# Performance work log

Measured on AMD Instinct MI355X. Metric: run time of the kernel, lower is better.

Reference implementation:

```python
import jax, jax.numpy as jnp
import numpy as np

B, T, N, SD, D, HYP, EMB = 128, 256, 8, 200, 64, 64, 32

def _ln(x, g, b, eps=1e-5):
    mu = jnp.mean(x, -1, keepdims=True)
    v = jnp.mean((x - mu) ** 2, -1, keepdims=True)
    return (x - mu) * jax.lax.rsqrt(v + eps) * g + b

def setup_inputs():
    key = jax.random.key(0)
    ks = iter(jax.random.split(key, 64))
    def p(shape, scale=0.05):
        return (jax.random.normal(next(ks), shape) * scale).astype(jnp.float32)
    n, sd, d, hyp, emb = N, SD, D, HYP, EMB
    return dict(
        qvals=p((B, T, n), 1.0), states=p((B, T, sd), 1.0), hidden_state=p((B, T, n, d), 1.0),
        enc_w1=p((sd, d)), enc_b1=p((d,)), enc_w2=p((d, d)), enc_b2=p((d,)),
        wq=p((d, d)), bq=p((d,)), wk=p((d, d)), bk=p((d,)), wv=p((d, d)), bv=p((d,)),
        wo=p((d, d)), bo=p((d,)),
        ln1_g=jnp.ones((d,), jnp.float32), ln1_b=jnp.zeros((d,), jnp.float32),
        ffn_w1=p((d, d)), ffn_b1=p((d,)), ffn_w2=p((d, d)), ffn_b2=p((d,)),
        ln2_g=jnp.ones((d,), jnp.float32), ln2_b=jnp.zeros((d,), jnp.float32),
        fc2ni_w=p((n, d, n - 1)), fc2ni_b=p((n, n - 1)),
        norm_g=jnp.ones((n - 1,), jnp.float32), norm_b=jnp.zeros((n - 1,), jnp.float32),
        w1a=p((2 * d, hyp)), b1a=p((hyp,)), w1b=p((hyp, n * emb)), b1b=p((n * emb,)),
        hb1w=p((2 * d, emb)), hb1b=p((emb,)),
        w2a=p((2 * d, hyp)), b2a=p((hyp,)), w2b=p((hyp, emb)), b2b=p((emb,)),
        hb2w1=p((2 * d, emb)), hb2b1=p((emb,)), hb2w2=p((emb, 1)), hb2b2=p((1,)))

def reference(qvals, states, hidden_state, enc_w1, enc_b1, enc_w2, enc_b2,
              wq, bq, wk, bk, wv, bv, wo, bo, ln1_g, ln1_b,
              ffn_w1, ffn_b1, ffn_w2, ffn_b2, ln2_g, ln2_b,
              fc2ni_w, fc2ni_b, norm_g, norm_b,
              w1a, b1a, w1b, b1b, hb1w, hb1b,
              w2a, b2a, w2b, b2b, hb2w1, hb2b1, hb2w2, hb2b2):
    sg = jax.lax.stop_gradient
    b, t, n = qvals.shape
    bt = b * t
    d = hidden_state.shape[-1]
    emb = hb1w.shape[1]
    # Encoder_s: relu(fc1) then tanh(fc2(e)+e)
    s = states.reshape(bt, -1)
    e = jax.nn.relu(s @ enc_w1 + enc_b1)
    enc = jnp.tanh(e @ enc_w2 + enc_b2 + e)                       # (bt, 64)
    # concat detached agent hiddens with detached state embedding -> (bt, n+1, 64)
    h = jnp.concatenate([sg(hidden_state.reshape(bt, n, d)), sg(enc)[:, None, :]], axis=1)
    # transformer block (single-head self-attention + FFN, post-LN)
    q = h @ wq + bq; k = h @ wk + bk; v = h @ wv + bv
    att = jax.nn.softmax(jnp.einsum('bid,bjd->bij', q, k) / jnp.sqrt(jnp.float32(d)), axis=-1)
    h2 = _ln(h + (att @ v) @ wo + bo, ln1_g, ln1_b)
    h3 = _ln(h2 + jax.nn.relu(h2 @ ffn_w1 + ffn_b1) @ ffn_w2 + ffn_b2, ln2_g, ln2_b)
    h_trans = h3[:, :n]                                           # (bt, n, 64)
    ens = jnp.concatenate([enc, sg(h_trans).mean(1)], axis=-1)    # (bt, 128)
    # per-agent fc2_Ni -> LayerNorm -> sigmoid, vectorized over agents
    ni = jnp.einsum('xnd,nde->xne', h_trans, fc2ni_w) + fc2ni_b   # (bt, n, n-1)
    ni = jax.nn.sigmoid(_ln(ni, norm_g, norm_b))
    # insert 1.0 at the diagonal (agent i keeps its own q with weight 1)
    rows = jnp.arange(n)[:, None]; cols = jnp.arange(n)[None, :]
    gidx = jnp.clip(cols - (cols > rows).astype(jnp.int32), 0, n - 2)  # (n, n)
    gathered = jnp.take_along_axis(ni, jnp.broadcast_to(gidx, (bt, n, n)), axis=-1)
    nfull = jnp.where(cols == rows, jnp.float32(1.0), gathered)   # (bt, n, n)
    N_nn = nfull.reshape(b, t, n, n)
    q_ni = (qvals[:, :, None, :] * N_nn).sum(-1).reshape(bt, 1, n)
    # hypernetwork mixing (QMIX)
    ens_d = sg(ens)
    w1 = jnp.abs(jax.nn.relu(ens_d @ w1a + b1a) @ w1b + b1b).reshape(bt, n, emb)
    b1 = (ens_d @ hb1w + hb1b).reshape(bt, 1, emb)
    w2 = jnp.abs(jax.nn.relu(ens @ w2a + b2a) @ w2b + b2b).reshape(bt, emb, 1)
    b2 = (jax.nn.relu(ens @ hb2w1 + hb2b1) @ hb2w2 + hb2b2).reshape(bt, 1, 1)
    hidden = jax.nn.elu(q_ni @ w1 + b1)
    y = (hidden @ w2 + b2).reshape(b, t, 1)
    eye_mask = jnp.broadcast_to(jnp.eye(n, dtype=bool), (b, t, n, n))
    return y, N_nn, eye_mask
```

## Files before the change

kernel.cpp:

```cpp
#include <hip/hip_runtime.h>
#include <hip/hip_bf16.h>

typedef __bf16 bf16x8 __attribute__((ext_vector_type(8)));
typedef __bf16 bf16x4 __attribute__((ext_vector_type(4)));
typedef float f32x4 __attribute__((ext_vector_type(4)));

#define ROWSG 32768
#define RB 8
#define HPAD 72
#define NN_OFF ((size_t)ROWSG)
#define EYE_OFF ((size_t)ROWSG + (size_t)ROWSG*64)

#define OFF_EW1   0
#define OFF_EW2   14336
#define OFF_WQ    18432
#define OFF_WK    22528
#define OFF_WV    26624
#define OFF_WO    30720
#define OFF_F1    34816
#define OFF_F2    38912
#define OFF_W1A   43008
#define OFF_W1B   51200
#define OFF_HB1W  67584
#define OFF_W2A   71680
#define OFF_W2B   79872
#define OFF_HB2W1 81920
#define WS_TOTAL  86016

__device__ __align__(16) __bf16 g_ws[WS_TOTAL];

#define MFMA16(a,b,c) __builtin_amdgcn_mfma_f32_16x16x32_bf16(a,b,c,0,0,0)

struct TP { const float* src[14]; };

__global__ __launch_bounds__(256) void wtrans(TP tp) {
    const int gid = blockIdx.x * 256 + threadIdx.x;
    if (gid >= WS_TOTAL) return;
    const int OFFS[14] = {OFF_EW1, OFF_EW2, OFF_WQ, OFF_WK, OFF_WV, OFF_WO, OFF_F1,
                          OFF_F2, OFF_W1A, OFF_W1B, OFF_HB1W, OFF_W2A, OFF_W2B, OFF_HB2W1};
    const int KPS[14]  = {224, 64, 64, 64, 64, 64, 64, 64, 128, 64, 128, 128, 64, 128};
    const int KRS[14]  = {200, 64, 64, 64, 64, 64, 64, 64, 128, 64, 128, 128, 64, 128};
    const int NS[14]   = {64, 64, 64, 64, 64, 64, 64, 64, 64, 256, 32, 64, 32, 32};
    int m = 0;
#pragma unroll
    for (int i = 1; i < 14; ++i) if (gid >= OFFS[i]) m = i;
    const int loc = gid - OFFS[m];
    const int Kp = KPS[m];
    const int n = loc / Kp;
    const int k = loc - n * Kp;
    float v = 0.f;
    if (k < KRS[m]) v = tp.src[m][(size_t)k * NS[m] + n];
    g_ws[gid] = (__bf16)v;
}

struct MainP {
    const float *qvals, *states, *hid, *eb1, *eb2, *bq, *bk, *bv, *bo,
        *l1g, *l1b, *fb1, *fb2, *l2g, *l2b, *niw, *nib, *ng, *nb,
        *b1a, *b1b, *hb1b, *b2a, *b2b, *hb2b1, *hw2, *hb2b2;
    float* out;
};

__device__ __forceinline__ void proj_ln(const __bf16* A, const __bf16* WT,
                                        const float* bias, const float* g, const float* bb,
                                        __bf16* H, int w, int quad, int l15) {
    for (int mti = 0; mti < 2; ++mti) {
        const int mt = w + 4 * mti;
        if (mt >= 5) continue;
        f32x4 acc0 = {0,0,0,0}, acc1 = {0,0,0,0}, acc2 = {0,0,0,0}, acc3 = {0,0,0,0};
#pragma unroll
        for (int ks = 0; ks < 2; ++ks) {
            const int kk = ks * 32 + quad * 8;
            const bf16x8 af = *(const bf16x8*)(A + (mt * 16 + l15) * HPAD + kk);
            acc0 = MFMA16(af, *(const bf16x8*)(WT + (size_t)(0 * 16 + l15) * 64 + kk), acc0);
            acc1 = MFMA16(af, *(const bf16x8*)(WT + (size_t)(1 * 16 + l15) * 64 + kk), acc1);
            acc2 = MFMA16(af, *(const bf16x8*)(WT + (size_t)(2 * 16 + l15) * 64 + kk), acc2);
            acc3 = MFMA16(af, *(const bf16x8*)(WT + (size_t)(3 * 16 + l15) * 64 + kk), acc3);
        }
        float v[4][4], g4[4], b4[4];
#pragma unroll
        for (int nt = 0; nt < 4; ++nt) {
            const int col = nt * 16 + l15;
            const float bo = bias[col];
            g4[nt] = g[col]; b4[nt] = bb[col];
            const f32x4 a = (nt == 0) ? acc0 : (nt == 1) ? acc1 : (nt == 2) ? acc2 : acc3;
#pragma unroll
            for (int r = 0; r < 4; ++r)
                v[nt][r] = a[r] + bo + (float)H[(mt * 16 + quad * 4 + r) * HPAD + col];
        }
#pragma unroll
        for (int r = 0; r < 4; ++r) {
            float s  = v[0][r] + v[1][r] + v[2][r] + v[3][r];
            float s2 = v[0][r]*v[0][r] + v[1][r]*v[1][r] + v[2][r]*v[2][r] + v[3][r]*v[3][r];
#pragma unroll
            for (int off = 1; off < 16; off <<= 1) {
                s  += __shfl_xor(s,  off, 64);
                s2 += __shfl_xor(s2, off, 64);
            }
            const float mu  = s * 0.015625f;
            const float var = s2 * 0.015625f - mu * mu;
            const float rs  = rsqrtf(var + 1e-5f);
#pragma unroll
            for (int nt = 0; nt < 4; ++nt)
                H[(mt * 16 + quad * 4 + r) * HPAD + nt * 16 + l15] =
                    (__bf16)((v[nt][r] - mu) * rs * g4[nt] + b4[nt]);
        }
    }
}

__global__ __launch_bounds__(256) void mixer_main(MainP p) {
    __shared__ __align__(16) __bf16 Hb[80 * HPAD];
    __shared__ __align__(16) __bf16 Qb[80 * HPAD];
    __shared__ __align__(16) __bf16 Kb[80 * HPAD];
    __shared__ __align__(16) __bf16 EbU[16 * HPAD];
    __shared__ __align__(16) __bf16 Tb2[16 * HPAD];
    __shared__ __align__(16) __bf16 ensB[16 * 136];
    __shared__ float  attU[8 * 81];
    __shared__ float  sQv[64];
    __shared__ float  qniL[64];
    __shared__ __align__(16) __bf16 W1bS[8 * 256];
    __shared__ float  B1f[8 * 32], W2f[8 * 32], T3f[8 * 32];

    const int blk = blockIdx.x;
    const int bt0 = blk * RB;
    const int t = threadIdx.x;
    const int w = t >> 6, lane = t & 63, quad = lane >> 4, l15 = lane & 15;
    const __bf16* ws = g_ws;
    __bf16* Sb = W1bS;

#pragma unroll
    for (int it = 0; it < 4; ++it) {
        const int u = it * 256 + t;
        const int x = u >> 7, rem = u & 127, n = rem >> 4, d4 = (rem & 15) * 4;
        const float4 v4 = *(const float4*)(p.hid + ((size_t)(bt0 + x) * 512 + n * 64 + d4));
        bf16x4 o; o[0] = (__bf16)v4.x; o[1] = (__bf16)v4.y; o[2] = (__bf16)v4.z; o[3] = (__bf16)v4.w;
        *(bf16x4*)(Hb + (x * 9 + n) * HPAD + d4) = o;
    }
#pragma unroll
    for (int it = 0; it < 2; ++it) {
        const int u = it * 256 + t;
        if (u < 400) {
            const int xr = u / 50, c4 = u - xr * 50;
            const float4 v4 = *(const float4*)(p.states + (size_t)(bt0 + xr) * 200 + c4 * 4);
            bf16x4 o; o[0] = (__bf16)v4.x; o[1] = (__bf16)v4.y; o[2] = (__bf16)v4.z; o[3] = (__bf16)v4.w;
            *(bf16x4*)(Sb + xr * 224 + c4 * 4) = o;
        }
    }
    if (t < 192) { const int xr = t / 24, c = t - xr * 24; Sb[xr * 224 + 200 + c] = (__bf16)0.0f; }
    if (t < 64) sQv[t] = p.qvals[(size_t)(bt0 + (t >> 3)) * 8 + (t & 7)];
    __syncthreads();

    float e4[4];
    {
        const int n0 = w * 16;
        const int srow = (l15 < 8) ? l15 : 7;
        f32x4 acc = {0, 0, 0, 0};
        for (int ks = 0; ks < 7; ++ks) {
            const int kk = ks * 32 + quad * 8;
            const bf16x8 af = *(const bf16x8*)(Sb + srow * 224 + kk);
            const bf16x8 bf = *(const bf16x8*)(ws + OFF_EW1 + (size_t)(n0 + l15) * 224 + kk);
            acc = MFMA16(af, bf, acc);
        }
        const float b1 = p.eb1[n0 + l15];
#pragma unroll
        for (int r = 0; r < 4; ++r) {
            const float ev = fmaxf(acc[r] + b1, 0.f);
            e4[r] = ev;
            EbU[(quad * 4 + r) * HPAD + n0 + l15] = (__bf16)ev;
        }
    }
    __syncthreads();

    {
        const int n0 = w * 16;
        f32x4 acc = {0, 0, 0, 0};
#pragma unroll
        for (int ks = 0; ks < 2; ++ks) {
            const int kk = ks * 32 + quad * 8;
            const bf16x8 af = *(const bf16x8*)(EbU + l15 * HPAD + kk);
            const bf16x8 bf = *(const bf16x8*)(ws + OFF_EW2 + (size_t)(n0 + l15) * 64 + kk);
            acc = MFMA16(af, bf, acc);
        }
        const float b2 = p.eb2[n0 + l15];
#pragma unroll
        for (int r = 0; r < 4; ++r) {
            const int xr = quad * 4 + r;
            if (xr < RB) {
                const float ev = tanhf(acc[r] + e4[r] + b2);
                Hb[(xr * 9 + 8) * HPAD + n0 + l15] = (__bf16)ev;
                ensB[xr * 136 + n0 + l15] = (__bf16)ev;
            }
        }
    }
    __syncthreads();

    for (int it = 0; it < 10; ++it) {
        const int j = w + 4 * it;
        const int mat = j / 20, r20 = j % 20, mt = r20 >> 2, nt = r20 & 3;
        const __bf16* wt = ws + (mat == 0 ? OFF_WQ : OFF_WK);
        const float* bias = (mat == 0 ? p.bq : p.bk);
        __bf16* dst = (mat == 0 ? Qb : Kb);
        f32x4 acc = {0, 0, 0, 0};
#pragma unroll
        for (int ks = 0; ks < 2; ++ks) {
            const int kk = ks * 32 + quad * 8;
            const bf16x8 af = *(const bf16x8*)(Hb + (mt * 16 + l15) * HPAD + kk);
            const bf16x8 bf = *(const bf16x8*)(wt + (size_t)(nt * 16 + l15) * 64 + kk);
            acc = MFMA16(af, bf, acc);
        }
        const float bv = bias[nt * 16 + l15];
#pragma unroll
        for (int r = 0; r < 4; ++r)
            dst[(mt * 16 + quad * 4 + r) * HPAD + nt * 16 + l15] = (__bf16)(acc[r] + bv);
    }
    __syncthreads();

    for (int xi = 0; xi < 2; ++xi) {
        const int x = w * 2 + xi;
        const int arow = (x * 9 + l15) * HPAD;
        f32x4 acc = {0, 0, 0, 0};
#pragma unroll
        for (int ks = 0; ks < 2; ++ks) {
            const int kk = ks * 32 + quad * 8;
            const bf16x8 qa = *(const bf16x8*)(Qb + arow + kk);
            const bf16x8 kb = *(const bf16x8*)(Kb + arow + kk);
            acc = MFMA16(qa, kb, acc);
        }
#pragma unroll
        for (int r = 0; r < 4; ++r) {
            const int i = quad * 4 + r;
            float s = (l15 < 9) ? acc[r] * 0.125f : -3.0e38f;
            float m = s;
#pragma unroll
            for (int off = 1; off < 16; off <<= 1) m = fmaxf(m, __shfl_xor(m, off, 64));
            float e = (l15 < 9) ? __expf(s - m) : 0.f;
            float sum = e;
#pragma unroll
            for (int off = 1; off < 16; off <<= 1) sum += __shfl_xor(sum, off, 64);
            const float pv = e / sum;
            if (i < 9 && l15 < 9) attU[x * 81 + i * 9 + l15] = pv;
        }
    }
    __syncthreads();

    for (int xi = 0; xi < 2; ++xi) {
        const int x = w * 2 + xi;
        float vreg[9];
#pragma unroll
        for (int jj = 0; jj < 9; ++jj) vreg[jj] = (float)Hb[(x * 9 + jj) * HPAD + lane];
#pragma unroll
        for (int i = 0; i < 9; ++i) {
            float a = 0.f;
#pragma unroll
            for (int jj = 0; jj < 9; ++jj) a += attU[x * 81 + i * 9 + jj] * vreg[jj];
            Kb[(x * 9 + i) * HPAD + lane] = (__bf16)a;
        }
    }
    __syncthreads();

    for (int it = 0; it < 5; ++it) {
        const int j = w + 4 * it;
        const int mt = j >> 2, nt = j & 3;
        f32x4 acc = {0, 0, 0, 0};
#pragma unroll
        for (int ks = 0; ks < 2; ++ks) {
            const int kk = ks * 32 + quad * 8;
            const bf16x8 af = *(const bf16x8*)(Kb + (mt * 16 + l15) * HPAD + kk);
            const bf16x8 bf = *(const bf16x8*)(ws + OFF_WV + (size_t)(nt * 16 + l15) * 64 + kk);
            acc = MFMA16(af, bf, acc);
        }
        const float bv = p.bv[nt * 16 + l15];
#pragma unroll
        for (int r = 0; r < 4; ++r)
            Qb[(mt * 16 + quad * 4 + r) * HPAD + nt * 16 + l15] = (__bf16)(acc[r] + bv);
    }
    __syncthreads();

    proj_ln(Qb, ws + OFF_WO, p.bo, p.l1g, p.l1b, Hb, w, quad, l15);
    __syncthreads();

    for (int it = 0; it < 5; ++it) {
        const int j = w + 4 * it;
        const int mt = j >> 2, nt = j & 3;
        f32x4 acc = {0, 0, 0, 0};
#pragma unroll
        for (int ks = 0; ks < 2; ++ks) {
            const int kk = ks * 32 + quad * 8;
            const bf16x8 af = *(const bf16x8*)(Hb + (mt * 16 + l15) * HPAD + kk);
            const bf16x8 bf = *(const bf16x8*)(ws + OFF_F1 + (size_t)(nt * 16 + l15) * 64 + kk);
            acc = MFMA16(af, bf, acc);
        }
        const float fb = p.fb1[nt * 16 + l15];
#pragma unroll
        for (int r = 0; r < 4; ++r)
            Kb[(mt * 16 + quad * 4 + r) * HPAD + nt * 16 + l15] = (__bf16)fmaxf(acc[r] + fb, 0.f);
    }
    __syncthreads();

    proj_ln(Kb, ws + OFF_F2, p.fb2, p.l2g, p.l2b, Hb, w, quad, l15);
    __syncthreads();

#pragma unroll
    for (int it = 0; it < 2; ++it) {
        const int id = it * 256 + t;
        const int x = id >> 6, col = id & 63;
        float s = 0.f;
#pragma unroll
        for (int i = 0; i < 8; ++i) s += (float)Hb[(x * 9 + i) * HPAD + col];
        ensB[x * 136 + 64 + col] = (__bf16)(s * 0.125f);
    }
    __syncthreads();

    {
        const int pr = t >> 2, q4 = t & 3;
        const int x = pr >> 3, n = pr & 7;
        float acc[7] = {0.f, 0.f, 0.f, 0.f, 0.f, 0.f, 0.f};
        const float* wni = p.niw + n * 448;
        for (int dd = 0; dd < 16; ++dd) {
            const int d = q4 * 16 + dd;
            const float hv = (float)Hb[(x * 9 + n) * HPAD + d];
#pragma unroll
            for (int e = 0; e < 7; ++e) acc[e] += hv * wni[d * 7 + e];
        }
#pragma unroll
        for (int e = 0; e < 7; ++e) {
            acc[e] += __shfl_xor(acc[e], 1, 64);
            acc[e] += __shfl_xor(acc[e], 2, 64);
        }
        if (q4 == 0) {
            float s = 0.f;
#pragma unroll
            for (int e = 0; e < 7; ++e) { acc[e] += p.nib[n * 7 + e]; s += acc[e]; }
            const float mu = s * (1.f / 7.f);
            float s2 = 0.f;
#pragma unroll
            for (int e = 0; e < 7; ++e) { const float d0 = acc[e] - mu; s2 += d0 * d0; }
            const float rs = rsqrtf(s2 * (1.f / 7.f) + 1e-5f);
            float* sNi = (float*)EbU;
#pragma unroll
            for (int e = 0; e < 7; ++e) {
                const float vv = (acc[e] - mu) * rs * p.ng[e] + p.nb[e];
                sNi[x * 64 + n * 8 + e] = 1.f / (1.f + __expf(-vv));
            }
        }
    }
    __syncthreads();

    {
        const float* sNi = (const float*)EbU;
        float* Nf = attU;
#pragma unroll
        for (int it = 0; it < 2; ++it) {
            const int id = it * 256 + t;
            const int x = id >> 6, rem = id & 63, i = rem >> 3, jj = rem & 7;
            const float nf = (i == jj) ? 1.f : sNi[x * 64 + i * 8 + (jj - (jj > i ? 1 : 0))];
            p.out[NN_OFF + (size_t)(bt0 + x) * 64 + rem] = nf;
            p.out[EYE_OFF + (size_t)(bt0 + x) * 64 + rem] = (i == jj) ? 1.f : 0.f;
            Nf[x * 64 + rem] = nf;
        }
    }
    __syncthreads();
    {
        const float* Nf = attU;
        const int pr = t >> 2, q4 = t & 3;
        const int x = pr >> 3, i = pr & 7;
        const int j0 = q4 * 2;
        float s = sQv[x * 8 + j0] * Nf[x * 64 + i * 8 + j0] +
                  sQv[x * 8 + j0 + 1] * Nf[x * 64 + i * 8 + j0 + 1];
        s += __shfl_xor(s, 1, 64);
        s += __shfl_xor(s, 2, 64);
        if (q4 == 0) qniL[x * 8 + i] = s;
    }
    __syncthreads();

    {
        const int n0 = w * 16;
#pragma unroll
        for (int m2 = 0; m2 < 2; ++m2) {
            const __bf16* wt = ws + (m2 == 0 ? OFF_W1A : OFF_W2A);
            const float* bias = m2 == 0 ? p.b1a : p.b2a;
            __bf16* dst = m2 == 0 ? EbU : Tb2;
            f32x4 acc = {0, 0, 0, 0};
#pragma unroll
            for (int ks = 0; ks < 4; ++ks) {
                const int kk = ks * 32 + quad * 8;
                const bf16x8 af = *(const bf16x8*)(ensB + l15 * 136 + kk);
                const bf16x8 bf = *(const bf16x8*)(wt + (size_t)(n0 + l15) * 128 + kk);
                acc = MFMA16(af, bf, acc);
            }
            const float bb = bias[n0 + l15];
#pragma unroll
            for (int r = 0; r < 4; ++r)
                dst[(quad * 4 + r) * HPAD + n0 + l15] = (__bf16)fmaxf(acc[r] + bb, 0.f);
        }
    }
    __syncthreads();

    for (int it = 0; it < 6; ++it) {
        const int j = w + 4 * it;
        if (j >= 22) continue;
        int mode, n0, Kp, ksteps, aStride;
        const __bf16 *A, *WT; const float* bias;
        if (j < 16)      { mode = 0; n0 = j * 16;        A = EbU;  aStride = HPAD; WT = ws + OFF_W1B;   bias = p.b1b;  Kp = 64;  ksteps = 2; }
        else if (j < 18) { mode = 1; n0 = (j - 16) * 16; A = ensB; aStride = 136;  WT = ws + OFF_HB1W;  bias = p.hb1b; Kp = 128; ksteps = 4; }
        else if (j < 20) { mode = 2; n0 = (j - 18) * 16; A = Tb2;  aStride = HPAD; WT = ws + OFF_W2B;   bias = p.b2b;  Kp = 64;  ksteps = 2; }
        else             { mode = 3; n0 = (j - 20) * 16; A = ensB; aStride = 136;  WT = ws + OFF_HB2W1; bias = p.hb2b1;Kp = 128; ksteps = 4; }
        f32x4 acc = {0, 0, 0, 0};
        for (int ks = 0; ks < ksteps; ++ks) {
            const int kk = ks * 32 + quad * 8;
            const bf16x8 af = *(const bf16x8*)(A + l15 * aStride + kk);
            const bf16x8 bf = *(const bf16x8*)(WT + (size_t)(n0 + l15) * Kp + kk);
            acc = MFMA16(af, bf, acc);
        }
        const float bb = bias[n0 + l15];
#pragma unroll
        for (int r = 0; r < 4; ++r) {
            const int xr = quad * 4 + r;
            if (xr < RB) {
                const float val = acc[r] + bb;
                if (mode == 0)      W1bS[xr * 256 + n0 + l15] = (__bf16)fabsf(val);
                else if (mode == 1) B1f[xr * 32 + n0 + l15] = val;
                else if (mode == 2) W2f[xr * 32 + n0 + l15] = fabsf(val);
                else                T3f[xr * 32 + n0 + l15] = fmaxf(val, 0.f);
            }
        }
    }
    __syncthreads();

    if (t < 128) {
        const int x = t >> 4, sub = t & 15;
        float pp = 0.f, pb = 0.f;
#pragma unroll
        for (int h2i = 0; h2i < 2; ++h2i) {
            const int e = sub + h2i * 16;
            float a = B1f[x * 32 + e];
#pragma unroll
            for (int i = 0; i < 8; ++i) a += qniL[x * 8 + i] * (float)W1bS[x * 256 + i * 32 + e];
            const float hid = a > 0.f ? a : (__expf(a) - 1.f);
            pp += hid * W2f[x * 32 + e];
            pb += T3f[x * 32 + e] * p.hw2[e];
        }
#pragma unroll
        for (int off = 1; off < 16; off <<= 1) {
            pp += __shfl_xor(pp, off, 64);
            pb += __shfl_xor(pb, off, 64);
        }
        if (sub == 0) p.out[bt0 + x] = pp + pb + p.hb2b2[0];
    }
}

extern "C" void kernel_launch(void* const* d_in, const int* in_sizes, int n_in,
                              void* d_out, int out_size, void* d_ws, size_t ws_size,
                              hipStream_t stream) {
    TP tp;
    tp.src[0]  = (const float*)d_in[3];
    tp.src[1]  = (const float*)d_in[5];
    tp.src[2]  = (const float*)d_in[7];
    tp.src[3]  = (const float*)d_in[9];
    tp.src[4]  = (const float*)d_in[11];
    tp.src[5]  = (const float*)d_in[13];
    tp.src[6]  = (const float*)d_in[17];
    tp.src[7]  = (const float*)d_in[19];
    tp.src[8]  = (const float*)d_in[27];
    tp.src[9]  = (const float*)d_in[29];
    tp.src[10] = (const float*)d_in[31];
    tp.src[11] = (const float*)d_in[33];
    tp.src[12] = (const float*)d_in[35];
    tp.src[13] = (const float*)d_in[37];
    wtrans<<<(WS_TOTAL + 255) / 256, 256, 0, stream>>>(tp);

    MainP p;
    p.qvals = (const float*)d_in[0];
    p.states = (const float*)d_in[1];
    p.hid = (const float*)d_in[2];
    p.eb1 = (const float*)d_in[4];
    p.eb2 = (const float*)d_in[6];
    p.bq = (const float*)d_in[8];
    p.bk = (const float*)d_in[10];
    p.bv = (const float*)d_in[12];
    p.bo = (const float*)d_in[14];
    p.l1g = (const float*)d_in[15];
    p.l1b = (const float*)d_in[16];
    p.fb1 = (const float*)d_in[18];
    p.fb2 = (const float*)d_in[20];
    p.l2g = (const float*)d_in[21];
    p.l2b = (const float*)d_in[22];
    p.niw = (const float*)d_in[23];
    p.nib = (const float*)d_in[24];
    p.ng = (const float*)d_in[25];
    p.nb = (const float*)d_in[26];
    p.b1a = (const float*)d_in[28];
    p.b1b = (const float*)d_in[30];
    p.hb1b = (const float*)d_in[32];
    p.b2a = (const float*)d_in[34];
    p.b2b = (const float*)d_in[36];
    p.hb2b1 = (const float*)d_in[38];
    p.hw2 = (const float*)d_in[39];
    p.hb2b2 = (const float*)d_in[40];
    p.out = (float*)d_out;

    mixer_main<<<ROWSG / RB, 256, 0, stream>>>(p);
}
```

Measured before the change: 436.9 us.

## Fold Wq·Wk into a single matrix and fuse per-tile projection chain

Attention scores are rewritten as H·(Wq Wkᵀ/8)·Hᵀ plus a per-key bias term. A small prep kernel precomputes the folded matrix and vector, which removes the separate K projection and the Kb buffer. The V, O+LN, FFN1 and FFN2+LN projections now run back to back per row tile inside each wave, and several block barriers and shared buffers are merged or dropped to cut shared memory and syncs. In exchange there is one more kernel launch and slightly different bf16 rounding of the scores.

After: 439.2 us. Within noise of the previous version (+0.5%).

```diff
diff --git a/kernel.cpp b/kernel.cpp
--- a/kernel.cpp
+++ b/kernel.cpp
@@ -26,8 +26,11 @@
 #define OFF_W2B   79872
 #define OFF_HB2W1 81920
 #define WS_TOTAL  86016
-
-__device__ __align__(16) __bf16 g_ws[WS_TOTAL];
+#define OFF_M     86016
+#define WS_TOTAL2 90112
+
+__device__ __align__(16) __bf16 g_ws[WS_TOTAL2];
+__device__ float g_v[64];
 
 #define MFMA16(a,b,c) __builtin_amdgcn_mfma_f32_16x16x32_bf16(a,b,c,0,0,0)
 
@@ -53,6 +56,25 @@
     g_ws[gid] = (__bf16)v;
 }
 
+struct PP { const float *wq, *wk, *bq; };
+
+__global__ __launch_bounds__(256) void wprep(PP pp) {
+    const int t = threadIdx.x;
+#pragma unroll 1
+    for (int q = 0; q < 16; ++q) {
+        const int idx = q * 256 + t;
+        const int f = idx >> 6, e = idx & 63;
+        float s = 0.f;
+        for (int n = 0; n < 64; ++n) s += pp.wq[e * 64 + n] * pp.wk[f * 64 + n];
+        g_ws[OFF_M + f * 64 + e] = (__bf16)(s * 0.125f);
+    }
+    if (t < 64) {
+        float s = 0.f;
+        for (int n = 0; n < 64; ++n) s += pp.wk[t * 64 + n] * pp.bq[n];
+        g_v[t] = s * 0.125f;
+    }
+}
+
 struct MainP {
     const float *qvals, *states, *hid, *eb1, *eb2, *bq, *bk, *bv, *bo,
         *l1g, *l1b, *fb1, *fb2, *l2g, *l2b, *niw, *nib, *ng, *nb,
@@ -60,49 +82,69 @@
     float* out;
 };
 
-__device__ __forceinline__ void proj_ln(const __bf16* A, const __bf16* WT,
-                                        const float* bias, const float* g, const float* bb,
-                                        __bf16* H, int w, int quad, int l15) {
-    for (int mti = 0; mti < 2; ++mti) {
-        const int mt = w + 4 * mti;
-        if (mt >= 5) continue;
-        f32x4 acc0 = {0,0,0,0}, acc1 = {0,0,0,0}, acc2 = {0,0,0,0}, acc3 = {0,0,0,0};
-#pragma unroll
-        for (int ks = 0; ks < 2; ++ks) {
-            const int kk = ks * 32 + quad * 8;
-            const bf16x8 af = *(const bf16x8*)(A + (mt * 16 + l15) * HPAD + kk);
-            acc0 = MFMA16(af, *(const bf16x8*)(WT + (size_t)(0 * 16 + l15) * 64 + kk), acc0);
-            acc1 = MFMA16(af, *(const bf16x8*)(WT + (size_t)(1 * 16 + l15) * 64 + kk), acc1);
-            acc2 = MFMA16(af, *(const bf16x8*)(WT + (size_t)(2 * 16 + l15) * 64 + kk), acc2);
-            acc3 = MFMA16(af, *(const bf16x8*)(WT + (size_t)(3 * 16 + l15) * 64 + kk), acc3);
-        }
-        float v[4][4], g4[4], b4[4];
-#pragma unroll
-        for (int nt = 0; nt < 4; ++nt) {
-            const int col = nt * 16 + l15;
-            const float bo = bias[col];
-            g4[nt] = g[col]; b4[nt] = bb[col];
-            const f32x4 a = (nt == 0) ? acc0 : (nt == 1) ? acc1 : (nt == 2) ? acc2 : acc3;
-#pragma unroll
-            for (int r = 0; r < 4; ++r)
-                v[nt][r] = a[r] + bo + (float)H[(mt * 16 + quad * 4 + r) * HPAD + col];
-        }
+__device__ __forceinline__ void proj_ln_tile(const __bf16* A, const __bf16* WT,
+                                             const float* bias, const float* g, const float* bb,
+                                             __bf16* H, int mt, int quad, int l15) {
+    f32x4 acc0 = {0,0,0,0}, acc1 = {0,0,0,0}, acc2 = {0,0,0,0}, acc3 = {0,0,0,0};
+#pragma unroll
+    for (int ks = 0; ks < 2; ++ks) {
+        const int kk = ks * 32 + quad * 8;
+        const bf16x8 af = *(const bf16x8*)(A + (mt * 16 + l15) * HPAD + kk);
+        acc0 = MFMA16(af, *(const bf16x8*)(WT + (size_t)(0 * 16 + l15) * 64 + kk), acc0);
+        acc1 = MFMA16(af, *(const bf16x8*)(WT + (size_t)(1 * 16 + l15) * 64 + kk), acc1);
+        acc2 = MFMA16(af, *(const bf16x8*)(WT + (size_t)(2 * 16 + l15) * 64 + kk), acc2);
+        acc3 = MFMA16(af, *(const bf16x8*)(WT + (size_t)(3 * 16 + l15) * 64 + kk), acc3);
+    }
+    float v[4][4], g4[4], b4[4];
+#pragma unroll
+    for (int nt = 0; nt < 4; ++nt) {
+        const int col = nt * 16 + l15;
+        const float bo = bias[col];
+        g4[nt] = g[col]; b4[nt] = bb[col];
+        const f32x4 a = (nt == 0) ? acc0 : (nt == 1) ? acc1 : (nt == 2) ? acc2 : acc3;
+#pragma unroll
+        for (int r = 0; r < 4; ++r)
+            v[nt][r] = a[r] + bo + (float)H[(mt * 16 + quad * 4 + r) * HPAD + col];
+    }
+#pragma unroll
+    for (int r = 0; r < 4; ++r) {
+        float s  = v[0][r] + v[1][r] + v[2][r] + v[3][r];
+        float s2 = v[0][r]*v[0][r] + v[1][r]*v[1][r] + v[2][r]*v[2][r] + v[3][r]*v[3][r];
+#pragma unroll
+        for (int off = 1; off < 16; off <<= 1) {
+            s  += __shfl_xor(s,  off, 64);
+            s2 += __shfl_xor(s2, off, 64);
+        }
+        const float mu  = s * 0.015625f;
+        const float var = s2 * 0.015625f - mu * mu;
+        const float rs  = rsqrtf(var + 1e-5f);
+#pragma unroll
+        for (int nt = 0; nt < 4; ++nt)
+            H[(mt * 16 + quad * 4 + r) * HPAD + nt * 16 + l15] =
+                (__bf16)((v[nt][r] - mu) * rs * g4[nt] + b4[nt]);
+    }
+}
+
+template<int ACT>
+__device__ __forceinline__ void proj_tile(const __bf16* A, const __bf16* WT, const float* bias,
+                                          __bf16* D, int mt, int quad, int l15) {
+    const int base = (mt * 16 + l15) * HPAD;
+    const bf16x8 a0 = *(const bf16x8*)(A + base + quad * 8);
+    const bf16x8 a1 = *(const bf16x8*)(A + base + 32 + quad * 8);
+    f32x4 acc[4] = {{0,0,0,0},{0,0,0,0},{0,0,0,0},{0,0,0,0}};
+#pragma unroll
+    for (int nt = 0; nt < 4; ++nt) {
+        acc[nt] = MFMA16(a0, *(const bf16x8*)(WT + (size_t)(nt * 16 + l15) * 64 + quad * 8), acc[nt]);
+        acc[nt] = MFMA16(a1, *(const bf16x8*)(WT + (size_t)(nt * 16 + l15) * 64 + 32 + quad * 8), acc[nt]);
+    }
+#pragma unroll
+    for (int nt = 0; nt < 4; ++nt) {
+        const float bv = bias[nt * 16 + l15];
 #pragma unroll
         for (int r = 0; r < 4; ++r) {
-            float s  = v[0][r] + v[1][r] + v[2][r] + v[3][r];
-            float s2 = v[0][r]*v[0][r] + v[1][r]*v[1][r] + v[2][r]*v[2][r] + v[3][r]*v[3][r];
-#pragma unroll
-            for (int off = 1; off < 16; off <<= 1) {
-                s  += __shfl_xor(s,  off, 64);
-                s2 += __shfl_xor(s2, off, 64);
-            }
-            const float mu  = s * 0.015625f;
-            const float var = s2 * 0.015625f - mu * mu;
-            const float rs  = rsqrtf(var + 1e-5f);
-#pragma unroll
-            for (int nt = 0; nt < 4; ++nt)
-                H[(mt * 16 + quad * 4 + r) * HPAD + nt * 16 + l15] =
-                    (__bf16)((v[nt][r] - mu) * rs * g4[nt] + b4[nt]);
+            float val = acc[nt][r] + bv;
+            if (ACT == 1) val = fmaxf(val, 0.f);
+            D[(mt * 16 + quad * 4 + r) * HPAD + nt * 16 + l15] = (__bf16)val;
         }
     }
 }
@@ -110,22 +152,27 @@
 __global__ __launch_bounds__(256) void mixer_main(MainP p) {
     __shared__ __align__(16) __bf16 Hb[80 * HPAD];
     __shared__ __align__(16) __bf16 Qb[80 * HPAD];
-    __shared__ __align__(16) __bf16 Kb[80 * HPAD];
     __shared__ __align__(16) __bf16 EbU[16 * HPAD];
     __shared__ __align__(16) __bf16 Tb2[16 * HPAD];
     __shared__ __align__(16) __bf16 ensB[16 * 136];
-    __shared__ float  attU[8 * 81];
-    __shared__ float  sQv[64];
-    __shared__ float  qniL[64];
+    __shared__ __align__(16) char   uniB[3072];
+    __shared__ float sQv[64];
+    __shared__ float qniL[64];
+    __shared__ float vhS[80];
     __shared__ __align__(16) __bf16 W1bS[8 * 256];
-    __shared__ float  B1f[8 * 32], W2f[8 * 32], T3f[8 * 32];
+
+    float* attU = (float*)uniB;
+    float* B1f  = (float*)uniB;
+    float* W2f  = (float*)(uniB + 1024);
+    float* T3f  = (float*)(uniB + 2048);
+    float* sNi  = (float*)W1bS;
+    __bf16* Sb  = W1bS;
 
     const int blk = blockIdx.x;
     const int bt0 = blk * RB;
     const int t = threadIdx.x;
     const int w = t >> 6, lane = t & 63, quad = lane >> 4, l15 = lane & 15;
     const __bf16* ws = g_ws;
-    __bf16* Sb = W1bS;
 
 #pragma unroll
     for (int it = 0; it < 4; ++it) {
@@ -193,24 +240,30 @@
     }
     __syncthreads();
 
-    for (int it = 0; it < 10; ++it) {
+    for (int it = 0; it < 5; ++it) {
         const int j = w + 4 * it;
-        const int mat = j / 20, r20 = j % 20, mt = r20 >> 2, nt = r20 & 3;
-        const __bf16* wt = ws + (mat == 0 ? OFF_WQ : OFF_WK);
-        const float* bias = (mat == 0 ? p.bq : p.bk);
-        __bf16* dst = (mat == 0 ? Qb : Kb);
+        const int mt = j >> 2, nt = j & 3;
         f32x4 acc = {0, 0, 0, 0};
 #pragma unroll
         for (int ks = 0; ks < 2; ++ks) {
             const int kk = ks * 32 + quad * 8;
             const bf16x8 af = *(const bf16x8*)(Hb + (mt * 16 + l15) * HPAD + kk);
-            const bf16x8 bf = *(const bf16x8*)(wt + (size_t)(nt * 16 + l15) * 64 + kk);
+            const bf16x8 bf = *(const bf16x8*)(ws + OFF_M + (size_t)(nt * 16 + l15) * 64 + kk);
             acc = MFMA16(af, bf, acc);
         }
-        const float bv = bias[nt * 16 + l15];
 #pragma unroll
         for (int r = 0; r < 4; ++r)
-            dst[(mt * 16 + quad * 4 + r) * HPAD + nt * 16 + l15] = (__bf16)(acc[r] + bv);
+            Qb[(mt * 16 + quad * 4 + r) * HPAD + nt * 16 + l15] = (__bf16)acc[r];
+    }
+    if (t < 72) {
+        float s = 0.f;
+#pragma unroll
+        for (int c8 = 0; c8 < 8; ++c8) {
+            const bf16x8 hv = *(const bf16x8*)(Hb + t * HPAD + c8 * 8);
+#pragma unroll
+            for (int jj = 0; jj < 8; ++jj) s += (float)hv[jj] * g_v[c8 * 8 + jj];
+        }
+        vhS[t] = s;
     }
     __syncthreads();
 
@@ -221,14 +274,13 @@
 #pragma unroll
         for (int ks = 0; ks < 2; ++ks) {
             const int kk = ks * 32 + quad * 8;
-            const bf16x8 qa = *(const bf16x8*)(Qb + arow + kk);
-            const bf16x8 kb = *(const bf16x8*)(Kb + arow + kk);
-            acc = MFMA16(qa, kb, acc);
-        }
+            acc = MFMA16(*(const bf16x8*)(Qb + arow + kk), *(const bf16x8*)(Hb + arow + kk), acc);
+        }
+        const float vh = (l15 < 9) ? vhS[x * 9 + l15] : 0.f;
 #pragma unroll
         for (int r = 0; r < 4; ++r) {
             const int i = quad * 4 + r;
-            float s = (l15 < 9) ? acc[r] * 0.125f : -3.0e38f;
+            float s = (l15 < 9) ? (acc[r] + vh) : -3.0e38f;
             float m = s;
 #pragma unroll
             for (int off = 1; off < 16; off <<= 1) m = fmaxf(m, __shfl_xor(m, off, 64));
@@ -236,14 +288,8 @@
             float sum = e;
 #pragma unroll
             for (int off = 1; off < 16; off <<= 1) sum += __shfl_xor(sum, off, 64);
-            const float pv = e / sum;
-            if (i < 9 && l15 < 9) attU[x * 81 + i * 9 + l15] = pv;
-        }
-    }
-    __syncthreads();
-
-    for (int xi = 0; xi < 2; ++xi) {
-        const int x = w * 2 + xi;
+            if (i < 9 && l15 < 9) attU[x * 81 + i * 9 + l15] = e / sum;
+        }
         float vreg[9];
 #pragma unroll
         for (int jj = 0; jj < 9; ++jj) vreg[jj] = (float)Hb[(x * 9 + jj) * HPAD + lane];
@@ -252,51 +298,19 @@
             float a = 0.f;
 #pragma unroll
             for (int jj = 0; jj < 9; ++jj) a += attU[x * 81 + i * 9 + jj] * vreg[jj];
-            Kb[(x * 9 + i) * HPAD + lane] = (__bf16)a;
-        }
-    }
-    __syncthreads();
-
-    for (int it = 0; it < 5; ++it) {
-        const int j = w + 4 * it;
-        const int mt = j >> 2, nt = j & 3;
-        f32x4 acc = {0, 0, 0, 0};
-#pragma unroll
-        for (int ks = 0; ks < 2; ++ks) {
-            const int kk = ks * 32 + quad * 8;
-            const bf16x8 af = *(const bf16x8*)(Kb + (mt * 16 + l15) * HPAD + kk);
-            const bf16x8 bf = *(const bf16x8*)(ws + OFF_WV + (size_t)(nt * 16 + l15) * 64 + kk);
-            acc = MFMA16(af, bf, acc);
-        }
-        const float bv = p.bv[nt * 16 + l15];
-#pragma unroll
-        for (int r = 0; r < 4; ++r)
-            Qb[(mt * 16 + quad * 4 + r) * HPAD + nt * 16 + l15] = (__bf16)(acc[r] + bv);
-    }
-    __syncthreads();
-
-    proj_ln(Qb, ws + OFF_WO, p.bo, p.l1g, p.l1b, Hb, w, quad, l15);
-    __syncthreads();
-
-    for (int it = 0; it < 5; ++it) {
-        const int j = w + 4 * it;
-        const int mt = j >> 2, nt = j & 3;
-        f32x4 acc = {0, 0, 0, 0};
-#pragma unroll
-        for (int ks = 0; ks < 2; ++ks) {
-            const int kk = ks * 32 + quad * 8;
-            const bf16x8 af = *(const bf16x8*)(Hb + (mt * 16 + l15) * HPAD + kk);
-            const bf16x8 bf = *(const bf16x8*)(ws + OFF_F1 + (size_t)(nt * 16 + l15) * 64 + kk);
-            acc = MFMA16(af, bf, acc);
-        }
-        const float fb = p.fb1[nt * 16 + l15];
-#pragma unroll
-        for (int r = 0; r < 4; ++r)
-            Kb[(mt * 16 + quad * 4 + r) * HPAD + nt * 16 + l15] = (__bf16)fmaxf(acc[r] + fb, 0.f);
-    }
-    __syncthreads();
-
-    proj_ln(Kb, ws + OFF_F2, p.fb2, p.l2g, p.l2b, Hb, w, quad, l15);
+            Qb[(x * 9 + i) * HPAD + lane] = (__bf16)a;
+        }
+    }
+    __syncthreads();
+
+    for (int mti = 0; mti < 2; ++mti) {
+        const int mt = w + 4 * mti;
+        if (mt >= 5) continue;
+        proj_tile<0>(Qb, ws + OFF_WV, p.bv, Qb, mt, quad, l15);
+        proj_ln_tile(Qb, ws + OFF_WO, p.bo, p.l1g, p.l1b, Hb, mt, quad, l15);
+        proj_tile<1>(Hb, ws + OFF_F1, p.fb1, Qb, mt, quad, l15);
+        proj_ln_tile(Qb, ws + OFF_F2, p.fb2, p.l2g, p.l2b, Hb, mt, quad, l15);
+    }
     __syncthreads();
 
 #pragma unroll
@@ -308,8 +322,6 @@
         for (int i = 0; i < 8; ++i) s += (float)Hb[(x * 9 + i) * HPAD + col];
         ensB[x * 136 + 64 + col] = (__bf16)(s * 0.125f);
     }
-    __syncthreads();
-
     {
         const int pr = t >> 2, q4 = t & 3;
         const int x = pr >> 3, n = pr & 7;
@@ -335,7 +347,6 @@
 #pragma unroll
             for (int e = 0; e < 7; ++e) { const float d0 = acc[e] - mu; s2 += d0 * d0; }
             const float rs = rsqrtf(s2 * (1.f / 7.f) + 1e-5f);
-            float* sNi = (float*)EbU;
 #pragma unroll
             for (int e = 0; e < 7; ++e) {
                 const float vv = (acc[e] - mu) * rs * p.ng[e] + p.nb[e];
@@ -345,33 +356,28 @@
     }
     __syncthreads();
 
+#pragma unroll
+    for (int it = 0; it < 2; ++it) {
+        const int id = it * 256 + t;
+        const int x = id >> 6, rem = id & 63, i = rem >> 3, jj = rem & 7;
+        const float nf = (i == jj) ? 1.f : sNi[x * 64 + i * 8 + (jj - (jj > i ? 1 : 0))];
+        p.out[NN_OFF + (size_t)(bt0 + x) * 64 + rem] = nf;
+        p.out[EYE_OFF + (size_t)(bt0 + x) * 64 + rem] = (i == jj) ? 1.f : 0.f;
+    }
     {
-        const float* sNi = (const float*)EbU;
-        float* Nf = attU;
-#pragma unroll
-        for (int it = 0; it < 2; ++it) {
-            const int id = it * 256 + t;
-            const int x = id >> 6, rem = id & 63, i = rem >> 3, jj = rem & 7;
-            const float nf = (i == jj) ? 1.f : sNi[x * 64 + i * 8 + (jj - (jj > i ? 1 : 0))];
-            p.out[NN_OFF + (size_t)(bt0 + x) * 64 + rem] = nf;
-            p.out[EYE_OFF + (size_t)(bt0 + x) * 64 + rem] = (i == jj) ? 1.f : 0.f;
-            Nf[x * 64 + rem] = nf;
-        }
-    }
-    __syncthreads();
-    {
-        const float* Nf = attU;
         const int pr = t >> 2, q4 = t & 3;
         const int x = pr >> 3, i = pr & 7;
-        const int j0 = q4 * 2;
-        float s = sQv[x * 8 + j0] * Nf[x * 64 + i * 8 + j0] +
-                  sQv[x * 8 + j0 + 1] * Nf[x * 64 + i * 8 + j0 + 1];
+        float s = 0.f;
+#pragma unroll
+        for (int jo = 0; jo < 2; ++jo) {
+            const int j = q4 * 2 + jo;
+            const float nf = (j == i) ? 1.f : sNi[x * 64 + i * 8 + (j - (j > i ? 1 : 0))];
+            s += sQv[x * 8 + j] * nf;
+        }
         s += __shfl_xor(s, 1, 64);
         s += __shfl_xor(s, 2, 64);
         if (q4 == 0) qniL[x * 8 + i] = s;
     }
-    __syncthreads();
-
     {
         const int n0 = w * 16;
 #pragma unroll
@@ -467,6 +473,12 @@
     tp.src[12] = (const float*)d_in[35];
     tp.src[13] = (const float*)d_in[37];
     wtrans<<<(WS_TOTAL + 255) / 256, 256, 0, stream>>>(tp);
+
+    PP pqk;
+    pqk.wq = (const float*)d_in[7];
+    pqk.wk = (const float*)d_in[9];
+    pqk.bq = (const float*)d_in[8];
+    wprep<<<1, 256, 0, stream>>>(pqk);
 
     MainP p;
     p.qvals = (const float*)d_in[0];
```
